# Kernel optimization log

Measured on AMD Instinct MI355X. Metric: run time of the kernel, lower is better.

## Reference

```python
import jax, jax.numpy as jnp
import numpy as np

CODEBOOK_SIZE = 8192
D_MODEL = 256
COMMITMENT_COST = 0.25


def setup_inputs() -> dict:
    key = jax.random.key(0)
    k1, k2 = jax.random.split(key)
    z = jax.random.normal(k1, (16, 512, D_MODEL), dtype=jnp.float32)
    # uniform(-1/K, 1/K) init like the torch module
    codebook = jax.random.uniform(
        k2, (CODEBOOK_SIZE, D_MODEL), dtype=jnp.float32,
        minval=-1.0 / CODEBOOK_SIZE, maxval=1.0 / CODEBOOK_SIZE)
    return {"z": z, "codebook": codebook}


def reference(z, codebook):
    B, P, D = z.shape
    flat = z.reshape(-1, D)  # [N, D]
    distances = (jnp.sum(flat * flat, axis=1, keepdims=True)
                 + jnp.sum(codebook * codebook, axis=1)
                 - 2.0 * jnp.matmul(flat, codebook.T))
    indices = jnp.argmin(distances, axis=1)  # [N] int
    quantized = codebook[indices]            # [N, D] gather
    # non-EMA VQ loss: codebook loss + commitment loss
    e_latent_loss = jnp.mean((jax.lax.stop_gradient(quantized) - flat) ** 2)
    q_latent_loss = jnp.mean((quantized - jax.lax.stop_gradient(flat)) ** 2)
    loss = q_latent_loss + COMMITMENT_COST * e_latent_loss
    # straight-through estimator
    quantized_st = flat + jax.lax.stop_gradient(quantized - flat)
    return (loss, quantized_st.reshape(B, P, D), indices.reshape(B, P))
```

## Files before the change

### kernel.cpp

```cpp
#include <hip/hip_runtime.h>
#include <hip/hip_bf16.h>
#include <math.h>


#define NROWS 8192
#define DDIM  256
#define KCW   8192
#define CAP   56
#define MARGIN 8e-4f

typedef __attribute__((ext_vector_type(8))) short short8;
typedef __attribute__((ext_vector_type(4))) float f32x4;
typedef unsigned int u32;

__device__ inline void async_copy16(void* lds_uniform, const void* gsrc) {
  __builtin_amdgcn_global_load_lds(
      (const __attribute__((address_space(1))) u32*)gsrc,
      (__attribute__((address_space(3))) u32*)lds_uniform, 16, 0, 0);
}

__device__ inline unsigned fmap(float f) {
  unsigned b = __float_as_uint(f);
  return (b & 0x80000000u) ? ~b : (b | 0x80000000u);
}
__device__ inline float funmap(unsigned u) {
  unsigned b = (u & 0x80000000u) ? (u & 0x7FFFFFFFu) : ~u;
  return __uint_as_float(b);
}

__global__ __launch_bounds__(256) void k_prep_cast(const float* __restrict__ z,
                                                   const float* __restrict__ cb,
                                                   ushort* __restrict__ zb,
                                                   ushort* __restrict__ cbb,
                                                   float* __restrict__ r2f,
                                                   float* __restrict__ e2f,
                                                   unsigned* __restrict__ rowMinU,
                                                   unsigned* __restrict__ cnt) {
  int t = threadIdx.x, w = t >> 6, lane = t & 63;
  int wid = blockIdx.x * 4 + w;
  bool isCb = wid >= NROWS;
  int row = isCb ? wid - NROWS : wid;
  const float* src = (isCb ? cb : z) + (size_t)row * DDIM + lane * 4;
  float4 v = *reinterpret_cast<const float4*>(src);
  ushort4 o;
  __hip_bfloat16 bx = __float2bfloat16(v.x); o.x = *(ushort*)&bx;
  __hip_bfloat16 by = __float2bfloat16(v.y); o.y = *(ushort*)&by;
  __hip_bfloat16 bz = __float2bfloat16(v.z); o.z = *(ushort*)&bz;
  __hip_bfloat16 bw = __float2bfloat16(v.w); o.w = *(ushort*)&bw;
  ushort* dst = (isCb ? cbb : zb) + (size_t)row * DDIM + lane * 4;
  *reinterpret_cast<ushort4*>(dst) = o;
  double d = (double)v.x * v.x + (double)v.y * v.y + (double)v.z * v.z + (double)v.w * v.w;
#pragma unroll
  for (int off = 1; off < 64; off <<= 1) d += __shfl_xor(d, off);
  if (lane == 0) {
    if (isCb) e2f[row] = (float)d;
    else { r2f[row] = (float)d; rowMinU[row] = ~0u; cnt[row] = 0; }
  }
}

template<int PHASE>
__global__ __launch_bounds__(256) void k_score(const ushort* __restrict__ zb,
                                               const ushort* __restrict__ cbb,
                                               const float* __restrict__ e2f,
                                               unsigned* __restrict__ rowMinU,
                                               unsigned* __restrict__ cnt,
                                               int* __restrict__ cand) {
  __shared__ ushort Ab[128 * 64];
  __shared__ ushort Bb[128 * 64];
  int t = threadIdx.x, w = t >> 6, lane = t & 63;
  int wg = ((blockIdx.x & 7) << 9) | (blockIdx.x >> 3);
  int mt = wg >> 6, nt = wg & 63;
  int wm = w >> 1, wn = w & 1;
  int cl = lane & 15, g = lane >> 4;

  int rloc8 = lane >> 3;
  int sslot = (lane & 7) ^ rloc8;
  const ushort* arow_base = zb  + (size_t)(mt * 128) * DDIM;
  const ushort* brow_base = cbb + (size_t)(nt * 128) * DDIM;

  f32x4 acc[4][4];
#pragma unroll
  for (int m = 0; m < 4; ++m)
#pragma unroll
    for (int n = 0; n < 4; ++n) acc[m][n] = (f32x4){0.f, 0.f, 0.f, 0.f};

  for (int ks = 0; ks < 4; ++ks) {
#pragma unroll
    for (int i = 0; i < 8; ++i) {
      int ch = w * 8 + i;
      int ct = ch & 15;
      int row = ct * 8 + rloc8;
      const ushort* src = (ch < 16)
          ? arow_base + (size_t)row * DDIM + ks * 64 + sslot * 8
          : brow_base + (size_t)row * DDIM + ks * 64 + sslot * 8;
      char* ldsb = (char*)(ch < 16 ? Ab : Bb) + ct * 1024;
      async_copy16(ldsb, src);
    }
    __syncthreads();
#pragma unroll
    for (int kk = 0; kk < 2; ++kk) {
      short8 af[4], bf[4];
#pragma unroll
      for (int m = 0; m < 4; ++m) {
        int arow = wm * 64 + m * 16 + cl;
        int ab = arow * 128 + (((kk * 4 + g) ^ (arow & 7)) << 4);
        af[m] = *reinterpret_cast<const short8*>((char*)Ab + ab);
      }
#pragma unroll
      for (int n = 0; n < 4; ++n) {
        int brow = wn * 64 + n * 16 + cl;
        int bb = brow * 128 + (((kk * 4 + g) ^ (brow & 7)) << 4);
        bf[n] = *reinterpret_cast<const short8*>((char*)Bb + bb);
      }
#pragma unroll
      for (int m = 0; m < 4; ++m)
#pragma unroll
        for (int n = 0; n < 4; ++n)
          acc[m][n] = __builtin_amdgcn_mfma_f32_16x16x32_bf16(af[m], bf[n], acc[m][n], 0, 0, 0);
    }
    __syncthreads();
  }

  int col_base = nt * 128 + wn * 64;
  int row_base = mt * 128 + wm * 64;
  float e2v[4];
#pragma unroll
  for (int n = 0; n < 4; ++n) e2v[n] = e2f[col_base + n * 16 + cl];

#pragma unroll
  for (int m = 0; m < 4; ++m) {
#pragma unroll
    for (int j = 0; j < 4; ++j) {
      int row = row_base + m * 16 + g * 4 + j;
      if (PHASE == 1) {
        float mn = INFINITY;
#pragma unroll
        for (int n = 0; n < 4; ++n) {
          float s = __fsub_rn(e2v[n], __fmul_rn(2.0f, acc[m][n][j]));
          mn = fminf(mn, s);
        }
#pragma unroll
        for (int off = 1; off < 16; off <<= 1)
          mn = fminf(mn, __shfl_xor(mn, off));
        if (cl == 0) atomicMin(&rowMinU[row], fmap(mn));
      } else {
        float thr = funmap(rowMinU[row]) + MARGIN;
#pragma unroll
        for (int n = 0; n < 4; ++n) {
          float s = __fsub_rn(e2v[n], __fmul_rn(2.0f, acc[m][n][j]));
          if (s <= thr) {
            unsigned slot = atomicAdd(&cnt[row], 1u);
            if (slot < CAP) cand[row * CAP + slot] = col_base + n * 16 + cl;
          }
        }
      }
    }
  }
}

__global__ __launch_bounds__(256) void k_rescore_gather(const float* __restrict__ z,
                                                        const float* __restrict__ cb,
                                                        const float* __restrict__ r2f,
                                                        const float* __restrict__ e2f,
                                                        const unsigned* __restrict__ cnt,
                                                        const int* __restrict__ cand,
                                                        float* __restrict__ out_q,
                                                        float* __restrict__ out_idx,
                                                        double* __restrict__ lpart) {
  int t = threadIdx.x, w = t >> 6, lane = t & 63;
  int row = blockIdx.x * 4 + w;
  unsigned n = cnt[row];
  float s = INFINITY; int ci = 0x7fffffff;
  const float* xp = z + (size_t)row * DDIM;
  float r2v = r2f[row];
  if (n <= CAP) {
    if (lane < (int)n) {
      ci = cand[row * CAP + lane];
      const float* ep = cb + (size_t)ci * DDIM;
      float acc = 0.f;
      for (int k = 0; k < DDIM; ++k) acc = __fmaf_rn(xp[k], ep[k], acc);
      s = __fsub_rn(__fadd_rn(r2v, e2f[ci]), __fmul_rn(2.0f, acc));
    }
  } else {
    for (int base = 0; base < KCW; base += 64) {
      int c = base + lane;
      const float* ep = cb + (size_t)c * DDIM;
      float acc = 0.f;
      for (int k = 0; k < DDIM; ++k) acc = __fmaf_rn(xp[k], ep[k], acc);
      float sc = __fsub_rn(__fadd_rn(r2v, e2f[c]), __fmul_rn(2.0f, acc));
      if (sc < s) { s = sc; ci = c; }
    }
  }
#pragma unroll
  for (int off = 1; off < 64; off <<= 1) {
    float os = __shfl_xor(s, off); int oi = __shfl_xor(ci, off);
    if (os < s || (os == s && oi < ci)) { s = os; ci = oi; }
  }
  if (lane == 0) out_idx[row] = (float)ci;

  float4 q = *reinterpret_cast<const float4*>(cb + (size_t)ci * DDIM + lane * 4);
  float4 x = *reinterpret_cast<const float4*>(xp + lane * 4);
  float* o = out_q + (size_t)row * DDIM + lane * 4;
  o[0] = q.x; o[1] = q.y; o[2] = q.z; o[3] = q.w;
  float dx = q.x - x.x, dy = q.y - x.y, dz = q.z - x.z, dw = q.w - x.w;
  double d = (double)dx * dx + (double)dy * dy + (double)dz * dz + (double)dw * dw;
#pragma unroll
  for (int off = 1; off < 64; off <<= 1) d += __shfl_xor(d, off);
  if (lane == 0) lpart[row] = d;
}

__global__ __launch_bounds__(256) void k_loss(const double* __restrict__ lpart,
                                              float* __restrict__ out0) {
  __shared__ double red[256];
  int t = threadIdx.x;
  double s = 0.0;
  for (int j = t; j < NROWS; j += 256) s += lpart[j];
  red[t] = s;
  __syncthreads();
  for (int off = 128; off > 0; off >>= 1) {
    if (t < off) red[t] += red[t + off];
    __syncthreads();
  }
  if (t == 0) out0[0] = (float)(1.25 * red[0] / (double)((size_t)NROWS * DDIM));
}

extern "C" void kernel_launch(void* const* d_in, const int* in_sizes, int n_in,
                              void* d_out, int out_size, void* d_ws, size_t ws_size,
                              hipStream_t stream) {
  const float* z  = (const float*)d_in[0];
  const float* cb = (const float*)d_in[1];
  float* out = (float*)d_out;
  char* ws = (char*)d_ws;
  const size_t HALF = (size_t)NROWS * DDIM;

  ushort* zb  = (ushort*)(out + 4);
  ushort* cbb = zb + HALF;

  size_t off = 0;
  float*    e2f     = (float*)(ws + off);    off += NROWS * 4;
  float*    r2f     = (float*)(ws + off);    off += NROWS * 4;
  unsigned* rowMinU = (unsigned*)(ws + off); off += NROWS * 4;
  unsigned* cnt     = (unsigned*)(ws + off); off += NROWS * 4;
  double*   lpart   = (double*)(ws + off);   off += NROWS * 8;
  int*      cand    = (int*)(ws + off);      off += (size_t)NROWS * CAP * 4;

  float* out_q   = out + 1;
  float* out_idx = out + 1 + HALF;

  k_prep_cast     <<<(2 * NROWS) / 4, 256, 0, stream>>>(z, cb, zb, cbb, r2f, e2f, rowMinU, cnt);
  k_score<1>      <<<64 * 64,         256, 0, stream>>>(zb, cbb, e2f, rowMinU, cnt, cand);
  k_score<2>      <<<64 * 64,         256, 0, stream>>>(zb, cbb, e2f, rowMinU, cnt, cand);
  k_rescore_gather<<<NROWS / 4,       256, 0, stream>>>(z, cb, r2f, e2f, cnt, cand, out_q, out_idx, lpart);
  k_loss          <<<1,               256, 0, stream>>>(lpart, out);
}
```

Before: 217.6 us.

## Replace two-pass bf16 scoring with single sweep using running per-row minimum

The two full GEMM passes (one for the row minimum, one for candidate collection) are merged into a single sweep kernel. Each block keeps 32 rows of A in registers, streams 128-column codebook tiles through LDS, and collects candidates against a running minimum held in shared memory. This removes one complete bf16 GEMM pass and the global rowMin array. Because the threshold only tightens over time, early tiles can emit more candidates, and with two column halves per row the minimum is only local to each half. CAP, MARGIN and the row-norm computation (now inside rescore) are also changed, so more rows may hit the slow full-rescore fallback.

```diff
diff --git a/kernel.cpp b/kernel.cpp
--- a/kernel.cpp
+++ b/kernel.cpp
@@ -6,8 +6,9 @@
 #define NROWS 8192
 #define DDIM  256
 #define KCW   8192
-#define CAP   56
-#define MARGIN 8e-4f
+#define CAP   64
+#define MARGIN 6e-4f
+#define TILES 32
 
 typedef __attribute__((ext_vector_type(8))) short short8;
 typedef __attribute__((ext_vector_type(4))) float f32x4;
@@ -32,9 +33,7 @@
                                                    const float* __restrict__ cb,
                                                    ushort* __restrict__ zb,
                                                    ushort* __restrict__ cbb,
-                                                   float* __restrict__ r2f,
                                                    float* __restrict__ e2f,
-                                                   unsigned* __restrict__ rowMinU,
                                                    unsigned* __restrict__ cnt) {
   int t = threadIdx.x, w = t >> 6, lane = t & 63;
   int wid = blockIdx.x * 4 + w;
@@ -49,130 +48,132 @@
   __hip_bfloat16 bw = __float2bfloat16(v.w); o.w = *(ushort*)&bw;
   ushort* dst = (isCb ? cbb : zb) + (size_t)row * DDIM + lane * 4;
   *reinterpret_cast<ushort4*>(dst) = o;
-  double d = (double)v.x * v.x + (double)v.y * v.y + (double)v.z * v.z + (double)v.w * v.w;
-#pragma unroll
-  for (int off = 1; off < 64; off <<= 1) d += __shfl_xor(d, off);
-  if (lane == 0) {
-    if (isCb) e2f[row] = (float)d;
-    else { r2f[row] = (float)d; rowMinU[row] = ~0u; cnt[row] = 0; }
-  }
-}
-
-template<int PHASE>
-__global__ __launch_bounds__(256) void k_score(const ushort* __restrict__ zb,
-                                               const ushort* __restrict__ cbb,
-                                               const float* __restrict__ e2f,
-                                               unsigned* __restrict__ rowMinU,
-                                               unsigned* __restrict__ cnt,
-                                               int* __restrict__ cand) {
-  __shared__ ushort Ab[128 * 64];
-  __shared__ ushort Bb[128 * 64];
+  if (isCb) {
+    double d = (double)v.x * v.x + (double)v.y * v.y + (double)v.z * v.z + (double)v.w * v.w;
+#pragma unroll
+    for (int off = 1; off < 64; off <<= 1) d += __shfl_xor(d, off);
+    if (lane == 0) e2f[row] = (float)d;
+  } else {
+    if (lane == 0) cnt[row] = 0;
+  }
+}
+
+__global__ __launch_bounds__(256, 2) void k_sweep(const ushort* __restrict__ zb,
+                                                  const ushort* __restrict__ cbb,
+                                                  const float* __restrict__ e2f,
+                                                  unsigned* __restrict__ cnt,
+                                                  int* __restrict__ cand) {
+  __shared__ ushort Bb[128 * 256];
+  __shared__ unsigned runmin[32];
   int t = threadIdx.x, w = t >> 6, lane = t & 63;
-  int wg = ((blockIdx.x & 7) << 9) | (blockIdx.x >> 3);
-  int mt = wg >> 6, nt = wg & 63;
-  int wm = w >> 1, wn = w & 1;
+  int wg = ((blockIdx.x & 7) << 6) | (blockIdx.x >> 3);
+  int rt = wg >> 1, h = wg & 1;
+  int R0 = rt * 32;
+  int C0 = h * 4096;
   int cl = lane & 15, g = lane >> 4;
 
-  int rloc8 = lane >> 3;
-  int sslot = (lane & 7) ^ rloc8;
-  const ushort* arow_base = zb  + (size_t)(mt * 128) * DDIM;
-  const ushort* brow_base = cbb + (size_t)(nt * 128) * DDIM;
-
-  f32x4 acc[4][4];
-#pragma unroll
-  for (int m = 0; m < 4; ++m)
-#pragma unroll
-    for (int n = 0; n < 4; ++n) acc[m][n] = (f32x4){0.f, 0.f, 0.f, 0.f};
-
-  for (int ks = 0; ks < 4; ++ks) {
-#pragma unroll
-    for (int i = 0; i < 8; ++i) {
-      int ch = w * 8 + i;
-      int ct = ch & 15;
-      int row = ct * 8 + rloc8;
-      const ushort* src = (ch < 16)
-          ? arow_base + (size_t)row * DDIM + ks * 64 + sslot * 8
-          : brow_base + (size_t)row * DDIM + ks * 64 + sslot * 8;
-      char* ldsb = (char*)(ch < 16 ? Ab : Bb) + ct * 1024;
-      async_copy16(ldsb, src);
-    }
+  if (t < 32) runmin[t] = ~0u;
+
+  short8 Areg[2][8];
+#pragma unroll
+  for (int m = 0; m < 2; ++m)
+#pragma unroll
+    for (int kk = 0; kk < 8; ++kk)
+      Areg[m][kk] = *reinterpret_cast<const short8*>(
+          &zb[(size_t)(R0 + m * 16 + cl) * DDIM + kk * 32 + g * 8]);
+  __syncthreads();
+
+  for (int tile = 0; tile < TILES; ++tile) {
+    int CT = C0 + tile * 128;
+#pragma unroll
+    for (int i = 0; i < 16; ++i) {
+      int col = i * 8 + w * 2 + (lane >> 5);
+      const ushort* src = cbb + (size_t)(CT + col) * DDIM + ((lane & 31) ^ (col & 7)) * 8;
+      char* dst = (char*)Bb + i * 4096 + w * 1024;
+      async_copy16(dst, src);
+    }
+    float e2v[2];
+#pragma unroll
+    for (int n = 0; n < 2; ++n) e2v[n] = e2f[CT + w * 32 + n * 16 + cl];
     __syncthreads();
-#pragma unroll
-    for (int kk = 0; kk < 2; ++kk) {
-      short8 af[4], bf[4];
-#pragma unroll
-      for (int m = 0; m < 4; ++m) {
-        int arow = wm * 64 + m * 16 + cl;
-        int ab = arow * 128 + (((kk * 4 + g) ^ (arow & 7)) << 4);
-        af[m] = *reinterpret_cast<const short8*>((char*)Ab + ab);
+
+    f32x4 acc[2][2];
+#pragma unroll
+    for (int m = 0; m < 2; ++m)
+#pragma unroll
+      for (int n = 0; n < 2; ++n) acc[m][n] = (f32x4){0.f, 0.f, 0.f, 0.f};
+#pragma unroll
+    for (int kk = 0; kk < 8; ++kk) {
+      short8 bfrag[2];
+#pragma unroll
+      for (int n = 0; n < 2; ++n) {
+        int col = w * 32 + n * 16 + cl;
+        int addr = col * 512 + (((kk * 4 + g) ^ (col & 7)) << 4);
+        bfrag[n] = *reinterpret_cast<const short8*>((char*)Bb + addr);
       }
 #pragma unroll
-      for (int n = 0; n < 4; ++n) {
-        int brow = wn * 64 + n * 16 + cl;
-        int bb = brow * 128 + (((kk * 4 + g) ^ (brow & 7)) << 4);
-        bf[n] = *reinterpret_cast<const short8*>((char*)Bb + bb);
+      for (int m = 0; m < 2; ++m)
+#pragma unroll
+        for (int n = 0; n < 2; ++n)
+          acc[m][n] = __builtin_amdgcn_mfma_f32_16x16x32_bf16(Areg[m][kk], bfrag[n], acc[m][n], 0, 0, 0);
+    }
+
+    float sc[2][2][4];
+#pragma unroll
+    for (int m = 0; m < 2; ++m)
+#pragma unroll
+      for (int n = 0; n < 2; ++n)
+#pragma unroll
+        for (int j = 0; j < 4; ++j)
+          sc[m][n][j] = __fsub_rn(e2v[n], __fmul_rn(2.0f, acc[m][n][j]));
+
+#pragma unroll
+    for (int m = 0; m < 2; ++m)
+#pragma unroll
+      for (int j = 0; j < 4; ++j) {
+        float mn = fminf(sc[m][0][j], sc[m][1][j]);
+#pragma unroll
+        for (int off = 1; off < 16; off <<= 1) mn = fminf(mn, __shfl_xor(mn, off));
+        if (cl == 0) atomicMin(&runmin[m * 16 + g * 4 + j], fmap(mn));
       }
 #pragma unroll
-      for (int m = 0; m < 4; ++m)
-#pragma unroll
-        for (int n = 0; n < 4; ++n)
-          acc[m][n] = __builtin_amdgcn_mfma_f32_16x16x32_bf16(af[m], bf[n], acc[m][n], 0, 0, 0);
-    }
-    __syncthreads();
-  }
-
-  int col_base = nt * 128 + wn * 64;
-  int row_base = mt * 128 + wm * 64;
-  float e2v[4];
-#pragma unroll
-  for (int n = 0; n < 4; ++n) e2v[n] = e2f[col_base + n * 16 + cl];
-
-#pragma unroll
-  for (int m = 0; m < 4; ++m) {
-#pragma unroll
-    for (int j = 0; j < 4; ++j) {
-      int row = row_base + m * 16 + g * 4 + j;
-      if (PHASE == 1) {
-        float mn = INFINITY;
-#pragma unroll
-        for (int n = 0; n < 4; ++n) {
-          float s = __fsub_rn(e2v[n], __fmul_rn(2.0f, acc[m][n][j]));
-          mn = fminf(mn, s);
-        }
-#pragma unroll
-        for (int off = 1; off < 16; off <<= 1)
-          mn = fminf(mn, __shfl_xor(mn, off));
-        if (cl == 0) atomicMin(&rowMinU[row], fmap(mn));
-      } else {
-        float thr = funmap(rowMinU[row]) + MARGIN;
-#pragma unroll
-        for (int n = 0; n < 4; ++n) {
-          float s = __fsub_rn(e2v[n], __fmul_rn(2.0f, acc[m][n][j]));
-          if (s <= thr) {
+    for (int m = 0; m < 2; ++m)
+#pragma unroll
+      for (int j = 0; j < 4; ++j) {
+        int rloc = m * 16 + g * 4 + j;
+        float thr = funmap(runmin[rloc]) + MARGIN;
+#pragma unroll
+        for (int n = 0; n < 2; ++n) {
+          if (sc[m][n][j] <= thr) {
+            int row = R0 + rloc;
             unsigned slot = atomicAdd(&cnt[row], 1u);
-            if (slot < CAP) cand[row * CAP + slot] = col_base + n * 16 + cl;
+            if (slot < CAP) cand[row * CAP + slot] = CT + w * 32 + n * 16 + cl;
           }
         }
       }
-    }
+    __syncthreads();
   }
 }
 
 __global__ __launch_bounds__(256) void k_rescore_gather(const float* __restrict__ z,
                                                         const float* __restrict__ cb,
-                                                        const float* __restrict__ r2f,
                                                         const float* __restrict__ e2f,
                                                         const unsigned* __restrict__ cnt,
                                                         const int* __restrict__ cand,
                                                         float* __restrict__ out_q,
                                                         float* __restrict__ out_idx,
-                                                        double* __restrict__ lpart) {
+                                                        float* __restrict__ lpart) {
   int t = threadIdx.x, w = t >> 6, lane = t & 63;
   int row = blockIdx.x * 4 + w;
+  const float* xp = z + (size_t)row * DDIM;
+  float4 x4 = *reinterpret_cast<const float4*>(xp + lane * 4);
+  double rd = (double)x4.x * x4.x + (double)x4.y * x4.y + (double)x4.z * x4.z + (double)x4.w * x4.w;
+#pragma unroll
+  for (int off = 1; off < 64; off <<= 1) rd += __shfl_xor(rd, off);
+  float r2v = (float)rd;
+
   unsigned n = cnt[row];
   float s = INFINITY; int ci = 0x7fffffff;
-  const float* xp = z + (size_t)row * DDIM;
-  float r2v = r2f[row];
   if (n <= CAP) {
     if (lane < (int)n) {
       ci = cand[row * CAP + lane];
@@ -187,8 +188,8 @@
       const float* ep = cb + (size_t)c * DDIM;
       float acc = 0.f;
       for (int k = 0; k < DDIM; ++k) acc = __fmaf_rn(xp[k], ep[k], acc);
-      float sc = __fsub_rn(__fadd_rn(r2v, e2f[c]), __fmul_rn(2.0f, acc));
-      if (sc < s) { s = sc; ci = c; }
+      float scv = __fsub_rn(__fadd_rn(r2v, e2f[c]), __fmul_rn(2.0f, acc));
+      if (scv < s) { s = scv; ci = c; }
     }
   }
 #pragma unroll
@@ -199,17 +200,16 @@
   if (lane == 0) out_idx[row] = (float)ci;
 
   float4 q = *reinterpret_cast<const float4*>(cb + (size_t)ci * DDIM + lane * 4);
-  float4 x = *reinterpret_cast<const float4*>(xp + lane * 4);
   float* o = out_q + (size_t)row * DDIM + lane * 4;
   o[0] = q.x; o[1] = q.y; o[2] = q.z; o[3] = q.w;
-  float dx = q.x - x.x, dy = q.y - x.y, dz = q.z - x.z, dw = q.w - x.w;
+  float dx = q.x - x4.x, dy = q.y - x4.y, dz = q.z - x4.z, dw = q.w - x4.w;
   double d = (double)dx * dx + (double)dy * dy + (double)dz * dz + (double)dw * dw;
 #pragma unroll
   for (int off = 1; off < 64; off <<= 1) d += __shfl_xor(d, off);
-  if (lane == 0) lpart[row] = d;
-}
-
-__global__ __launch_bounds__(256) void k_loss(const double* __restrict__ lpart,
+  if (lane == 0) lpart[row] = (float)d;
+}
+
+__global__ __launch_bounds__(256) void k_loss(const float* __restrict__ lpart,
                                               float* __restrict__ out0) {
   __shared__ double red[256];
   int t = threadIdx.x;
@@ -237,19 +237,16 @@
   ushort* cbb = zb + HALF;
 
   size_t off = 0;
-  float*    e2f     = (float*)(ws + off);    off += NROWS * 4;
-  float*    r2f     = (float*)(ws + off);    off += NROWS * 4;
-  unsigned* rowMinU = (unsigned*)(ws + off); off += NROWS * 4;
-  unsigned* cnt     = (unsigned*)(ws + off); off += NROWS * 4;
-  double*   lpart   = (double*)(ws + off);   off += NROWS * 8;
-  int*      cand    = (int*)(ws + off);      off += (size_t)NROWS * CAP * 4;
+  float*    e2f   = (float*)(ws + off);    off += NROWS * 4;
+  unsigned* cnt   = (unsigned*)(ws + off); off += NROWS * 4;
+  float*    lpart = (float*)(ws + off);    off += NROWS * 4;
+  int*      cand  = (int*)(ws + off);      off += (size_t)NROWS * CAP * 4;
 
   float* out_q   = out + 1;
   float* out_idx = out + 1 + HALF;
 
-  k_prep_cast     <<<(2 * NROWS) / 4, 256, 0, stream>>>(z, cb, zb, cbb, r2f, e2f, rowMinU, cnt);
-  k_score<1>      <<<64 * 64,         256, 0, stream>>>(zb, cbb, e2f, rowMinU, cnt, cand);
-  k_score<2>      <<<64 * 64,         256, 0, stream>>>(zb, cbb, e2f, rowMinU, cnt, cand);
-  k_rescore_gather<<<NROWS / 4,       256, 0, stream>>>(z, cb, r2f, e2f, cnt, cand, out_q, out_idx, lpart);
+  k_prep_cast     <<<(2 * NROWS) / 4, 256, 0, stream>>>(z, cb, zb, cbb, e2f, cnt);
+  k_sweep         <<<512,             256, 0, stream>>>(zb, cbb, e2f, cnt, cand);
+  k_rescore_gather<<<NROWS / 4,       256, 0, stream>>>(z, cb, e2f, cnt, cand, out_q, out_idx, lpart);
   k_loss          <<<1,               256, 0, stream>>>(lpart, out);
 }
```

Result: no change. 220.6 us (+1.4%).

## Merge two-pass scoring into a single pass with running-min candidate capture

Applied to the files above, without the earlier changes.

Drops the second bf16 GEMM pass. The single scoring kernel now takes a running row minimum through atomicMin and immediately records candidates within a margin of min(old, local min). Candidate indices shrink to ushort and CAP grows to 128, so more candidates pass through while the running minimum is still loose. The rescore step now computes the row norm itself with float4 loads, and the loss partials and rowMinU share one workspace buffer. The cost is more atomics and more rescoring work from early, weak thresholds, plus a fallback to a full scan whenever a row overflows CAP.

```diff
diff --git a/kernel.cpp b/kernel.cpp
--- a/kernel.cpp
+++ b/kernel.cpp
@@ -6,8 +6,8 @@
 #define NROWS 8192
 #define DDIM  256
 #define KCW   8192
-#define CAP   56
-#define MARGIN 8e-4f
+#define CAP   128
+#define MARGIN 5e-4f
 
 typedef __attribute__((ext_vector_type(8))) short short8;
 typedef __attribute__((ext_vector_type(4))) float f32x4;
@@ -32,7 +32,6 @@
                                                    const float* __restrict__ cb,
                                                    ushort* __restrict__ zb,
                                                    ushort* __restrict__ cbb,
-                                                   float* __restrict__ r2f,
                                                    float* __restrict__ e2f,
                                                    unsigned* __restrict__ rowMinU,
                                                    unsigned* __restrict__ cnt) {
@@ -49,22 +48,22 @@
   __hip_bfloat16 bw = __float2bfloat16(v.w); o.w = *(ushort*)&bw;
   ushort* dst = (isCb ? cbb : zb) + (size_t)row * DDIM + lane * 4;
   *reinterpret_cast<ushort4*>(dst) = o;
-  double d = (double)v.x * v.x + (double)v.y * v.y + (double)v.z * v.z + (double)v.w * v.w;
-#pragma unroll
-  for (int off = 1; off < 64; off <<= 1) d += __shfl_xor(d, off);
-  if (lane == 0) {
-    if (isCb) e2f[row] = (float)d;
-    else { r2f[row] = (float)d; rowMinU[row] = ~0u; cnt[row] = 0; }
-  }
-}
-
-template<int PHASE>
-__global__ __launch_bounds__(256) void k_score(const ushort* __restrict__ zb,
-                                               const ushort* __restrict__ cbb,
-                                               const float* __restrict__ e2f,
-                                               unsigned* __restrict__ rowMinU,
-                                               unsigned* __restrict__ cnt,
-                                               int* __restrict__ cand) {
+  if (isCb) {
+    double d = (double)v.x * v.x + (double)v.y * v.y + (double)v.z * v.z + (double)v.w * v.w;
+#pragma unroll
+    for (int off = 1; off < 64; off <<= 1) d += __shfl_xor(d, off);
+    if (lane == 0) e2f[row] = (float)d;
+  } else {
+    if (lane == 0) { rowMinU[row] = ~0u; cnt[row] = 0; }
+  }
+}
+
+__global__ __launch_bounds__(256) void k_score1(const ushort* __restrict__ zb,
+                                                const ushort* __restrict__ cbb,
+                                                const float* __restrict__ e2f,
+                                                unsigned* __restrict__ rowMinU,
+                                                unsigned* __restrict__ cnt,
+                                                ushort* __restrict__ cand) {
   __shared__ ushort Ab[128 * 64];
   __shared__ ushort Bb[128 * 64];
   int t = threadIdx.x, w = t >> 6, lane = t & 63;
@@ -132,63 +131,83 @@
 #pragma unroll
     for (int j = 0; j < 4; ++j) {
       int row = row_base + m * 16 + g * 4 + j;
-      if (PHASE == 1) {
-        float mn = INFINITY;
-#pragma unroll
-        for (int n = 0; n < 4; ++n) {
-          float s = __fsub_rn(e2v[n], __fmul_rn(2.0f, acc[m][n][j]));
-          mn = fminf(mn, s);
-        }
-#pragma unroll
-        for (int off = 1; off < 16; off <<= 1)
-          mn = fminf(mn, __shfl_xor(mn, off));
-        if (cl == 0) atomicMin(&rowMinU[row], fmap(mn));
-      } else {
-        float thr = funmap(rowMinU[row]) + MARGIN;
-#pragma unroll
-        for (int n = 0; n < 4; ++n) {
-          float s = __fsub_rn(e2v[n], __fmul_rn(2.0f, acc[m][n][j]));
-          if (s <= thr) {
-            unsigned slot = atomicAdd(&cnt[row], 1u);
-            if (slot < CAP) cand[row * CAP + slot] = col_base + n * 16 + cl;
-          }
-        }
-      }
+      float s0 = __fsub_rn(e2v[0], __fmul_rn(2.0f, acc[m][0][j]));
+      float s1 = __fsub_rn(e2v[1], __fmul_rn(2.0f, acc[m][1][j]));
+      float s2 = __fsub_rn(e2v[2], __fmul_rn(2.0f, acc[m][2][j]));
+      float s3 = __fsub_rn(e2v[3], __fmul_rn(2.0f, acc[m][3][j]));
+      float mn = fminf(fminf(s0, s1), fminf(s2, s3));
+#pragma unroll
+      for (int off = 1; off < 16; off <<= 1)
+        mn = fminf(mn, __shfl_xor(mn, off));
+      float thr;
+      if (cl == 0) {
+        unsigned old = atomicMin(&rowMinU[row], fmap(mn));
+        thr = fminf(funmap(old), mn) + MARGIN;
+      }
+      thr = __shfl(thr, g << 4);
+      if (s0 <= thr) { unsigned sl = atomicAdd(&cnt[row], 1u); if (sl < CAP) cand[(size_t)row * CAP + sl] = (ushort)(col_base + 0 * 16 + cl); }
+      if (s1 <= thr) { unsigned sl = atomicAdd(&cnt[row], 1u); if (sl < CAP) cand[(size_t)row * CAP + sl] = (ushort)(col_base + 1 * 16 + cl); }
+      if (s2 <= thr) { unsigned sl = atomicAdd(&cnt[row], 1u); if (sl < CAP) cand[(size_t)row * CAP + sl] = (ushort)(col_base + 2 * 16 + cl); }
+      if (s3 <= thr) { unsigned sl = atomicAdd(&cnt[row], 1u); if (sl < CAP) cand[(size_t)row * CAP + sl] = (ushort)(col_base + 3 * 16 + cl); }
     }
   }
 }
 
 __global__ __launch_bounds__(256) void k_rescore_gather(const float* __restrict__ z,
                                                         const float* __restrict__ cb,
-                                                        const float* __restrict__ r2f,
                                                         const float* __restrict__ e2f,
                                                         const unsigned* __restrict__ cnt,
-                                                        const int* __restrict__ cand,
+                                                        const ushort* __restrict__ cand,
                                                         float* __restrict__ out_q,
                                                         float* __restrict__ out_idx,
-                                                        double* __restrict__ lpart) {
+                                                        float* __restrict__ lpart) {
   int t = threadIdx.x, w = t >> 6, lane = t & 63;
   int row = blockIdx.x * 4 + w;
+  const float* xp = z + (size_t)row * DDIM;
+  const float4* xp4 = reinterpret_cast<const float4*>(xp);
+  float4 x4 = xp4[lane];
+  double rd = (double)x4.x * x4.x + (double)x4.y * x4.y + (double)x4.z * x4.z + (double)x4.w * x4.w;
+#pragma unroll
+  for (int off = 1; off < 64; off <<= 1) rd += __shfl_xor(rd, off);
+  float r2v = (float)rd;
+
   unsigned n = cnt[row];
   float s = INFINITY; int ci = 0x7fffffff;
-  const float* xp = z + (size_t)row * DDIM;
-  float r2v = r2f[row];
   if (n <= CAP) {
-    if (lane < (int)n) {
-      ci = cand[row * CAP + lane];
-      const float* ep = cb + (size_t)ci * DDIM;
-      float acc = 0.f;
-      for (int k = 0; k < DDIM; ++k) acc = __fmaf_rn(xp[k], ep[k], acc);
-      s = __fsub_rn(__fadd_rn(r2v, e2f[ci]), __fmul_rn(2.0f, acc));
+#pragma unroll
+    for (int base = 0; base < CAP; base += 64) {
+      int k_i = base + lane;
+      if (k_i < (int)n) {
+        int c = cand[(size_t)row * CAP + k_i];
+        const float4* ep4 = reinterpret_cast<const float4*>(cb + (size_t)c * DDIM);
+        float acc = 0.f;
+#pragma unroll 4
+        for (int k4 = 0; k4 < 64; ++k4) {
+          float4 e = ep4[k4], x = xp4[k4];
+          acc = __fmaf_rn(x.x, e.x, acc);
+          acc = __fmaf_rn(x.y, e.y, acc);
+          acc = __fmaf_rn(x.z, e.z, acc);
+          acc = __fmaf_rn(x.w, e.w, acc);
+        }
+        float scv = __fsub_rn(__fadd_rn(r2v, e2f[c]), __fmul_rn(2.0f, acc));
+        if (scv < s || (scv == s && c < ci)) { s = scv; ci = c; }
+      }
     }
   } else {
     for (int base = 0; base < KCW; base += 64) {
       int c = base + lane;
-      const float* ep = cb + (size_t)c * DDIM;
+      const float4* ep4 = reinterpret_cast<const float4*>(cb + (size_t)c * DDIM);
       float acc = 0.f;
-      for (int k = 0; k < DDIM; ++k) acc = __fmaf_rn(xp[k], ep[k], acc);
-      float sc = __fsub_rn(__fadd_rn(r2v, e2f[c]), __fmul_rn(2.0f, acc));
-      if (sc < s) { s = sc; ci = c; }
+#pragma unroll 4
+      for (int k4 = 0; k4 < 64; ++k4) {
+        float4 e = ep4[k4], x = xp4[k4];
+        acc = __fmaf_rn(x.x, e.x, acc);
+        acc = __fmaf_rn(x.y, e.y, acc);
+        acc = __fmaf_rn(x.z, e.z, acc);
+        acc = __fmaf_rn(x.w, e.w, acc);
+      }
+      float scv = __fsub_rn(__fadd_rn(r2v, e2f[c]), __fmul_rn(2.0f, acc));
+      if (scv < s) { s = scv; ci = c; }
     }
   }
 #pragma unroll
@@ -198,18 +217,17 @@
   }
   if (lane == 0) out_idx[row] = (float)ci;
 
-  float4 q = *reinterpret_cast<const float4*>(cb + (size_t)ci * DDIM + lane * 4);
-  float4 x = *reinterpret_cast<const float4*>(xp + lane * 4);
+  float4 qv = *reinterpret_cast<const float4*>(cb + (size_t)ci * DDIM + lane * 4);
   float* o = out_q + (size_t)row * DDIM + lane * 4;
-  o[0] = q.x; o[1] = q.y; o[2] = q.z; o[3] = q.w;
-  float dx = q.x - x.x, dy = q.y - x.y, dz = q.z - x.z, dw = q.w - x.w;
+  o[0] = qv.x; o[1] = qv.y; o[2] = qv.z; o[3] = qv.w;
+  float dx = qv.x - x4.x, dy = qv.y - x4.y, dz = qv.z - x4.z, dw = qv.w - x4.w;
   double d = (double)dx * dx + (double)dy * dy + (double)dz * dz + (double)dw * dw;
 #pragma unroll
   for (int off = 1; off < 64; off <<= 1) d += __shfl_xor(d, off);
-  if (lane == 0) lpart[row] = d;
-}
-
-__global__ __launch_bounds__(256) void k_loss(const double* __restrict__ lpart,
+  if (lane == 0) lpart[row] = (float)d;
+}
+
+__global__ __launch_bounds__(256) void k_loss(const float* __restrict__ lpart,
                                               float* __restrict__ out0) {
   __shared__ double red[256];
   int t = threadIdx.x;
@@ -238,18 +256,16 @@
 
   size_t off = 0;
   float*    e2f     = (float*)(ws + off);    off += NROWS * 4;
-  float*    r2f     = (float*)(ws + off);    off += NROWS * 4;
-  unsigned* rowMinU = (unsigned*)(ws + off); off += NROWS * 4;
   unsigned* cnt     = (unsigned*)(ws + off); off += NROWS * 4;
-  double*   lpart   = (double*)(ws + off);   off += NROWS * 8;
-  int*      cand    = (int*)(ws + off);      off += (size_t)NROWS * CAP * 4;
+  unsigned* rowMinU = (unsigned*)(ws + off);
+  float*    lpart   = (float*)(ws + off);    off += NROWS * 4;
+  ushort*   cand    = (ushort*)(ws + off);   off += (size_t)NROWS * CAP * 2;
 
   float* out_q   = out + 1;
   float* out_idx = out + 1 + HALF;
 
-  k_prep_cast     <<<(2 * NROWS) / 4, 256, 0, stream>>>(z, cb, zb, cbb, r2f, e2f, rowMinU, cnt);
-  k_score<1>      <<<64 * 64,         256, 0, stream>>>(zb, cbb, e2f, rowMinU, cnt, cand);
-  k_score<2>      <<<64 * 64,         256, 0, stream>>>(zb, cbb, e2f, rowMinU, cnt, cand);
-  k_rescore_gather<<<NROWS / 4,       256, 0, stream>>>(z, cb, r2f, e2f, cnt, cand, out_q, out_idx, lpart);
+  k_prep_cast     <<<(2 * NROWS) / 4, 256, 0, stream>>>(z, cb, zb, cbb, e2f, rowMinU, cnt);
+  k_score1        <<<64 * 64,         256, 0, stream>>>(zb, cbb, e2f, rowMinU, cnt, cand);
+  k_rescore_gather<<<NROWS / 4,       256, 0, stream>>>(z, cb, e2f, cnt, cand, out_q, out_idx, lpart);
   k_loss          <<<1,               256, 0, stream>>>(lpart, out);
 }
```

Measured after the change: 246.3 us. 13.2% more time.
